# Optimization experiments

Hardware: AMD Instinct MI355X
Metric: run time of the kernel (lower is better)

Reference implementation:

```python
import jax, jax.numpy as jnp
import numpy as np

N = 50000      # total nodes
E = 800000     # total edges (before self-loops)
B = 512        # graphs in batch
H = 4          # attention heads
D = 64         # per-head dim (hidden 256 = H*D)
F_IN = 203     # node feature dim
HID = H * D
NEG_SLOPE = 0.2  # PyG GATConv LeakyReLU default
LN_EPS = 1e-5


def setup_inputs() -> dict:
    key = jax.random.key(0)
    ks = jax.random.split(key, 24)
    g = lambda k, shape, fan: (jax.random.normal(k, shape, jnp.float32) / np.sqrt(fan))
    inp = {
        "x": jax.random.normal(ks[0], (N, F_IN), jnp.float32),
        "edge_index": jax.random.randint(ks[1], (2, E), 0, N, jnp.int64),
        "edge_weight": jax.random.uniform(ks[2], (E,), jnp.float32),
        "batch": jnp.sort(jax.random.randint(ks[3], (N,), 0, B, jnp.int64)),
        # GAT layer 1 params
        "W1": g(ks[4], (HID, F_IN), F_IN),
        "a_s1": g(ks[5], (H, D), D),
        "a_d1": g(ks[6], (H, D), D),
        "a_e1": g(ks[7], (H, D), D),
        "We1": g(ks[8], (HID, 1), 1),
        "b1": jnp.zeros((HID,), jnp.float32),
        # GAT layer 2 params
        "W2": g(ks[9], (HID, HID), HID),
        "a_s2": g(ks[10], (H, D), D),
        "a_d2": g(ks[11], (H, D), D),
        "a_e2": g(ks[12], (H, D), D),
        "We2": g(ks[13], (HID, 1), 1),
        "b2": jnp.zeros((HID,), jnp.float32),
        # LayerNorms
        "ln1_g": jnp.ones((HID,), jnp.float32),
        "ln1_b": jnp.zeros((HID,), jnp.float32),
        "ln2_g": jnp.ones((HID,), jnp.float32),
        "ln2_b": jnp.zeros((HID,), jnp.float32),
    }
    return inp


def _gat(x, src, dst, e_attr, W, a_s, a_d, a_e, We, bias, n_nodes):
    # projected node features: [N, H, D]
    xp = (x @ W.T).reshape(n_nodes, H, D)
    alpha_src = jnp.einsum('nhd,hd->nh', xp, a_s)   # [N, H]
    alpha_dst = jnp.einsum('nhd,hd->nh', xp, a_d)   # [N, H]
    ep = (e_attr @ We.T).reshape(-1, H, D)          # [E', H, D]
    alpha_edge = jnp.einsum('ehd,hd->eh', ep, a_e)  # [E', H]
    logits = jax.nn.leaky_relu(alpha_src[src] + alpha_dst[dst] + alpha_edge, NEG_SLOPE)
    # segment softmax over incoming edges per destination node
    m = jax.ops.segment_max(logits, dst, num_segments=n_nodes)
    ex = jnp.exp(logits - m[dst])
    denom = jax.ops.segment_sum(ex, dst, num_segments=n_nodes)
    alpha = ex / denom[dst]                          # [E', H]
    msg = alpha[:, :, None] * xp[src]                # [E', H, D]
    out = jax.ops.segment_sum(msg, dst, num_segments=n_nodes)
    return out.reshape(n_nodes, HID) + bias


def _ln(x, g, b):
    mu = x.mean(-1, keepdims=True)
    var = ((x - mu) ** 2).mean(-1, keepdims=True)
    return (x - mu) * jax.lax.rsqrt(var + LN_EPS) * g + b


def reference(x, edge_index, edge_weight, batch,
              W1, a_s1, a_d1, a_e1, We1, b1,
              W2, a_s2, a_d2, a_e2, We2, b2,
              ln1_g, ln1_b, ln2_g, ln2_b):
    n = x.shape[0]
    # PyG GATConv add_self_loops=True, edge_attr fill_value='mean'
    loop = jnp.arange(n)
    src = jnp.concatenate([edge_index[0], loop])
    dst = jnp.concatenate([edge_index[1], loop])
    ew = jnp.concatenate([edge_weight, jnp.full((n,), edge_weight.mean(), edge_weight.dtype)])
    e_attr = ew[:, None]  # edge_dim = 1

    h = _gat(x, src, dst, e_attr, W1, a_s1, a_d1, a_e1, We1, b1, n)
    h = jax.nn.elu(_ln(h, ln1_g, ln1_b))  # dropout omitted (eval mode)
    h = _gat(h, src, dst, e_attr, W2, a_s2, a_d2, a_e2, We2, b2, n)
    h = jax.nn.elu(_ln(h, ln2_g, ln2_b))

    # global_mean_pool
    s = jax.ops.segment_sum(h, batch, num_segments=B)
    cnt = jax.ops.segment_sum(jnp.ones((n,), h.dtype), batch, num_segments=B)
    return s / jnp.maximum(cnt, 1.0)[:, None]
```

## Files before the change

kernel.cpp:

```cpp
#include <hip/hip_runtime.h>
#include <math.h>

#define HID 256
#define NEG_SLOPE 0.2f
#define LN_EPS 1e-5f
#define BINCAP 127

typedef __attribute__((ext_vector_type(4))) float f32x4;
typedef __attribute__((ext_vector_type(8))) short bf16x8;
typedef __attribute__((address_space(3))) unsigned char lds_b;
typedef const __attribute__((address_space(1))) unsigned char glob_b;

__device__ __forceinline__ float bf2f_lo(unsigned int u) {
    union { unsigned int i; float f; } c; c.i = u << 16; return c.f;
}
__device__ __forceinline__ float bf2f_hi(unsigned int u) {
    union { unsigned int i; float f; } c; c.i = u & 0xffff0000u; return c.f;
}
__device__ __forceinline__ float bf2f_u(unsigned short u) {
    union { unsigned int i; float f; } c; c.i = ((unsigned int)u) << 16; return c.f;
}
__device__ __forceinline__ unsigned short f2bf(float f) {
    union { float f; unsigned int i; } c; c.f = f;
    unsigned int i = c.i;
    return (unsigned short)((i + 0x7fffu + ((i >> 16) & 1u)) >> 16);
}

__global__ __launch_bounds__(256) void k_pre(const float* __restrict__ ew, int E,
                                             const int* __restrict__ ei, int N, int EN, int NH,
                                             float* __restrict__ partials,
                                             int* __restrict__ bins, int* __restrict__ spill, int* __restrict__ spill_cnt,
                                             const float* __restrict__ W1, const float* __restrict__ W2,
                                             unsigned short* __restrict__ o1, unsigned short* __restrict__ o2, int K1,
                                             const float* __restrict__ x, unsigned short* __restrict__ x16, int FIN) {
    int t = threadIdx.x;
    int b = blockIdx.x;
    if (b < NH) {
        int i = b * 1024 + t;
#pragma unroll
        for (int c = 0; c < 4; c++) {
            int e = i + c * 256;
            if (e < EN) {
                int d = (e < E) ? ei[E + e] : (e - E);
                int* row = bins + (size_t)d * 128;
                int pos = atomicAdd(row, 1);
                if (pos < BINCAP) row[1 + pos] = e;
                else { int q = atomicAdd(spill_cnt, 1); spill[2 * q] = d; spill[2 * q + 1] = e; }
            }
        }
    } else if (b < NH + 256) {
        __shared__ float sdata[4];
        int sb = b - NH;
        float v = 0.f;
        for (int i = sb * 256 + t; i < E; i += 65536) v += ew[i];
        for (int o = 32; o; o >>= 1) v += __shfl_xor(v, o);
        if ((t & 63) == 0) sdata[t >> 6] = v;
        __syncthreads();
        if (t == 0) partials[sb] = sdata[0] + sdata[1] + sdata[2] + sdata[3];
    } else if (b < NH + 256 + 512) {
        int wb = b - NH - 256;
        const float* in = (wb < 256) ? W1 : W2;
        unsigned short* out = (wb < 256) ? o1 : o2;
        int K = (wb < 256) ? K1 : 256;
        int col = wb & 255;
        float v = (t < K) ? in[(size_t)col * K + t] : 0.f;
        int ks = t >> 5, j = (t >> 3) & 3, e = t & 7;
        out[ks * 8192 + j * 2048 + ((((col << 4) ^ (j << 4))) >> 1) + e] = f2bf(v);
    } else {
        int r = b - NH - 256 - 512;
        x16[(size_t)r * 256 + t] = (t < FIN) ? f2bf(x[(size_t)r * FIN + t]) : (unsigned short)0;
    }
}

__global__ __launch_bounds__(256) void k_scanred_coeff(const int* __restrict__ bins, int N, int NB,
                                                       int* __restrict__ deg_dense, int* __restrict__ bsum,
                                                       const float* __restrict__ partials, float* __restrict__ sumw,
                                                       const float* __restrict__ We1, const float* __restrict__ ae1,
                                                       const float* __restrict__ We2, const float* __restrict__ ae2,
                                                       float* __restrict__ c1, float* __restrict__ c2) {
    int t = threadIdx.x;
    int b = blockIdx.x;
    if (b < NB) {
        __shared__ int sdata[4];
        int i = b * 256 + t;
        int v = (i < N) ? bins[(size_t)i * 128] : 0;
        if (i < N) deg_dense[i] = v;
        for (int o = 32; o; o >>= 1) v += __shfl_xor(v, o);
        if ((t & 63) == 0) sdata[t >> 6] = v;
        __syncthreads();
        if (t == 0) bsum[b] = sdata[0] + sdata[1] + sdata[2] + sdata[3];
    } else if (b == NB) {
        __shared__ float sdata[4];
        float v = partials[t];
        for (int o = 32; o; o >>= 1) v += __shfl_xor(v, o);
        if ((t & 63) == 0) sdata[t >> 6] = v;
        __syncthreads();
        if (t == 0) *sumw = sdata[0] + sdata[1] + sdata[2] + sdata[3];
    } else {
        float v1 = We1[t] * ae1[t];
        float v2 = We2[t] * ae2[t];
        for (int o = 1; o < 64; o <<= 1) { v1 += __shfl_xor(v1, o); v2 += __shfl_xor(v2, o); }
        if ((t & 63) == 0) { c1[t >> 6] = v1; c2[t >> 6] = v2; }
    }
}

__global__ __launch_bounds__(256) void k_scan_apply(const int* __restrict__ deg, int N, int NB,
                                                    const int* __restrict__ bsum, int* __restrict__ offs) {
    __shared__ int sm[256];
    __shared__ int sb[256];
    int t = threadIdx.x;
    int i = blockIdx.x * 256 + t;
    int v = (i < N) ? deg[i] : 0;
    int vb = (t < NB) ? bsum[t] : 0;
    sm[t] = v;
    sb[t] = vb;
    __syncthreads();
    for (int o = 1; o < 256; o <<= 1) {
        int tv = (t >= o) ? sm[t - o] : 0;
        int tb = (t >= o) ? sb[t - o] : 0;
        __syncthreads();
        sm[t] += tv;
        sb[t] += tb;
        __syncthreads();
    }
    int myb = bsum[blockIdx.x];
    int boff = sb[blockIdx.x] - myb;
    if (i < N) {
        offs[i] = boff + sm[t] - v;
        if (i == N - 1) offs[N] = boff + sm[t];
    }
}

__device__ __forceinline__ void gemm_dev(int bid,
    const unsigned short* __restrict__ A16, const unsigned short* __restrict__ Bt16, int M,
    const float* __restrict__ asf, const float* __restrict__ adf,
    unsigned short* __restrict__ C16, float* __restrict__ as_out, float* __restrict__ ad_out)
{
    __shared__ __align__(16) unsigned short Bsl[4 * 256 * 8];
    int t = threadIdx.x;
    int lane = t & 63, w = t >> 6;
    int row0 = bid << 5;
    int kg = lane >> 4, fr = lane & 15;

    int ar0 = row0 + fr;      if (ar0 >= M) ar0 = 0;
    int ar1 = row0 + 16 + fr; if (ar1 >= M) ar1 = 0;
    const unsigned short* ap0 = A16 + (size_t)ar0 * 256 + (kg << 3);
    const unsigned short* ap1 = A16 + (size_t)ar1 * 256 + (kg << 3);

    f32x4 acc[2][4];
#pragma unroll
    for (int i = 0; i < 2; i++)
#pragma unroll
        for (int j = 0; j < 4; j++) acc[i][j] = (f32x4){0.f, 0.f, 0.f, 0.f};

    for (int ks = 0; ks < 8; ks++) {
#pragma unroll
        for (int j = 0; j < 4; j++) {
            __builtin_amdgcn_global_load_lds(
                (glob_b*)(Bt16 + (size_t)ks * 8192 + j * 2048 + t * 8),
                (lds_b*)((char*)Bsl + j * 4096 + t * 16),
                16, 0, 0);
        }
        bf16x8 a0 = *(const bf16x8*)(ap0 + (ks << 5));
        bf16x8 a1 = *(const bf16x8*)(ap1 + (ks << 5));
        __syncthreads();
#pragma unroll
        for (int nf = 0; nf < 4; nf++) {
            int col = (w << 6) + (nf << 4) + fr;
            bf16x8 bv = *(const bf16x8*)((const char*)Bsl + (kg << 12) + (((col << 4)) ^ (kg << 4)));
            acc[0][nf] = __builtin_amdgcn_mfma_f32_16x16x32_bf16(a0, bv, acc[0][nf], 0, 0, 0);
            acc[1][nf] = __builtin_amdgcn_mfma_f32_16x16x32_bf16(a1, bv, acc[1][nf], 0, 0, 0);
        }
        __syncthreads();
    }

#pragma unroll
    for (int mf = 0; mf < 2; mf++)
#pragma unroll
        for (int j = 0; j < 4; j++) {
            int gr = row0 + mf * 16 + kg * 4 + j;
            if (gr < M) {
#pragma unroll
                for (int nf = 0; nf < 4; nf++)
                    C16[(size_t)gr * 256 + (w << 6) + (nf << 4) + fr] = f2bf(acc[mf][nf][j]);
            }
        }
    float asv[4], adv[4];
#pragma unroll
    for (int nf = 0; nf < 4; nf++) {
        int col = (w << 6) + (nf << 4) + fr;
        asv[nf] = asf[col]; adv[nf] = adf[col];
    }
#pragma unroll
    for (int mf = 0; mf < 2; mf++)
#pragma unroll
        for (int j = 0; j < 4; j++) {
            float ps = acc[mf][0][j] * asv[0] + acc[mf][1][j] * asv[1] + acc[mf][2][j] * asv[2] + acc[mf][3][j] * asv[3];
            float pd = acc[mf][0][j] * adv[0] + acc[mf][1][j] * adv[1] + acc[mf][2][j] * adv[2] + acc[mf][3][j] * adv[3];
#pragma unroll
            for (int o = 1; o < 16; o <<= 1) { ps += __shfl_xor(ps, o); pd += __shfl_xor(pd, o); }
            if (fr == 0) {
                int gr = row0 + mf * 16 + kg * 4 + j;
                if (gr < M) {
                    as_out[gr * 4 + w] = ps;
                    ad_out[gr * 4 + w] = pd;
                }
            }
        }
}

__device__ __forceinline__ void compact_dev(int bid, const int* __restrict__ offs,
                                            const int* __restrict__ bins,
                                            const int* __restrict__ spill, const int* __restrict__ spill_cnt,
                                            const int* __restrict__ ei, const float* __restrict__ ew,
                                            const float* __restrict__ sumw, int E, int N,
                                            int* __restrict__ csr_src, float* __restrict__ csr_w) {
    int lane = threadIdx.x & 63;
    int n = (bid << 2) + (threadIdx.x >> 6);
    if (n >= N) return;
    int s0 = offs[n];
    int d = offs[n + 1] - s0;
    if (d <= 0) return;
    if (d <= 64) {
        int key = (lane < d) ? bins[(size_t)n * 128 + 1 + lane] : 0x7fffffff;
        int rank = 0;
        for (int j = 0; j < d; j++) {
            int kj = __shfl(key, j);
            rank += (kj < key) ? 1 : 0;
        }
        if (lane < d) {
            int s; float wv;
            if (key < E) { s = ei[key]; wv = ew[key]; }
            else         { s = key - E; wv = *sumw / (float)E; }
            csr_src[s0 + rank] = s;
            csr_w[s0 + rank] = wv;
        }
    } else {
        if (lane == 0) {
            int m = (d < BINCAP) ? d : BINCAP;
            for (int i = 0; i < m; i++) csr_src[s0 + i] = bins[(size_t)n * 128 + 1 + i];
            int cnt = m;
            int st = *spill_cnt;
            for (int k = 0; k < st; k++)
                if (spill[2 * k] == n) csr_src[s0 + cnt++] = spill[2 * k + 1];
            for (int i = s0 + 1; i < s0 + d; i++) {
                int ke = csr_src[i];
                int j = i - 1;
                while (j >= s0 && csr_src[j] > ke) { csr_src[j + 1] = csr_src[j]; j--; }
                csr_src[j + 1] = ke;
            }
        }
        __threadfence();
        __builtin_amdgcn_wave_barrier();
        for (int i = lane; i < d; i += 64) {
            int e = csr_src[s0 + i];
            int s; float wv;
            if (e < E) { s = ei[e]; wv = ew[e]; }
            else       { s = e - E; wv = *sumw / (float)E; }
            csr_src[s0 + i] = s;
            csr_w[s0 + i] = wv;
        }
    }
}

__global__ __launch_bounds__(256) void k_gemm_sort(int MB,
    const unsigned short* __restrict__ A16, const unsigned short* __restrict__ Bt16, int M,
    const float* __restrict__ asf, const float* __restrict__ adf,
    unsigned short* __restrict__ C16, float* __restrict__ as_out, float* __restrict__ ad_out,
    const int* __restrict__ offs, const int* __restrict__ bins,
    const int* __restrict__ spill, const int* __restrict__ spill_cnt,
    const int* __restrict__ ei, const float* __restrict__ ew,
    const float* __restrict__ sumw, int E,
    int* __restrict__ csr_src, float* __restrict__ csr_w) {
    if ((int)blockIdx.x < MB)
        gemm_dev(blockIdx.x, A16, Bt16, M, asf, adf, C16, as_out, ad_out);
    else
        compact_dev(blockIdx.x - MB, offs, bins, spill, spill_cnt, ei, ew, sumw, E, M, csr_src, csr_w);
}

__global__ __launch_bounds__(256) void gemm_mfma(
    const unsigned short* __restrict__ A16, const unsigned short* __restrict__ Bt16, int M,
    const float* __restrict__ asf, const float* __restrict__ adf,
    unsigned short* __restrict__ C16, float* __restrict__ as_out, float* __restrict__ ad_out) {
    gemm_dev(blockIdx.x, A16, Bt16, M, asf, adf, C16, as_out, ad_out);
}

#define ACC8V(u, q) do { \
    f32x4 va = { bf2f_lo((u).x), bf2f_hi((u).x), bf2f_lo((u).y), bf2f_hi((u).y) }; \
    f32x4 vb = { bf2f_lo((u).z), bf2f_hi((u).z), bf2f_lo((u).w), bf2f_hi((u).w) }; \
    accA += va * (q); accB += vb * (q); } while (0)

__global__ __launch_bounds__(256) void gat_kernel(
    const unsigned short* __restrict__ xp16, const int* __restrict__ offs,
    const int* __restrict__ csr_src, const float* __restrict__ csr_w,
    const float* __restrict__ as_, const float* __restrict__ ad_,
    const float* __restrict__ cvec, const float* __restrict__ bias,
    const float* __restrict__ ln_g, const float* __restrict__ ln_b,
    int N, unsigned short* __restrict__ out16) {
    __shared__ float p_lds[4][256];
    __shared__ int   s_lds[4][64];
    int lane = threadIdx.x & 63;
    int wid = threadIdx.x >> 6;
    int n = (blockIdx.x << 2) + wid;
    if (n >= N) return;
    int start = offs[n], end = offs[n + 1];
    int e0 = lane >> 5;
    int colb = lane & 31;
    int hq2 = colb >> 3;
    const unsigned short* xbase = xp16 + (size_t)colb * 8;
    float4 adv = *(const float4*)(ad_ + (size_t)n * 4);
    float c0 = cvec[0], c1 = cvec[1], c2 = cvec[2], c3 = cvec[3];
    float dn = 0.f;
    f32x4 accA = (f32x4){0.f, 0.f, 0.f, 0.f};
    f32x4 accB = (f32x4){0.f, 0.f, 0.f, 0.f};

    for (int base = start; base < end; base += 64) {
        int idx = base + lane;
        bool act = idx < end;
        int s = act ? csr_src[idx] : 0;
        float w = act ? csr_w[idx] : 0.f;
        float4 av = *(const float4*)(as_ + (size_t)s * 4);
        float l0 = av.x + adv.x + w * c0; l0 = l0 >= 0.f ? l0 : NEG_SLOPE * l0;
        float l1 = av.y + adv.y + w * c1; l1 = l1 >= 0.f ? l1 : NEG_SLOPE * l1;
        float l2 = av.z + adv.z + w * c2; l2 = l2 >= 0.f ? l2 : NEG_SLOPE * l2;
        float l3 = av.w + adv.w + w * c3; l3 = l3 >= 0.f ? l3 : NEG_SLOPE * l3;
        float p0 = act ? __expf(fminf(l0, 80.f)) : 0.f;
        float p1 = act ? __expf(fminf(l1, 80.f)) : 0.f;
        float p2 = act ? __expf(fminf(l2, 80.f)) : 0.f;
        float p3 = act ? __expf(fminf(l3, 80.f)) : 0.f;
        float4 pv = { p0, p1, p2, p3 };
        *(float4*)&p_lds[wid][lane << 2] = pv;
        s_lds[wid][lane] = s;
        int cnt = end - base; if (cnt > 64) cnt = 64;
        int k = 0;
        for (; k + 8 <= cnt; k += 8) {
            int i0 = k + e0, i1 = k + 2 + e0, i2 = k + 4 + e0, i3 = k + 6 + e0;
            int s0 = s_lds[wid][i0], s1 = s_lds[wid][i1], s2 = s_lds[wid][i2], s3 = s_lds[wid][i3];
            uint4 u0 = *(const uint4*)(xbase + (size_t)s0 * 256);
            uint4 u1 = *(const uint4*)(xbase + (size_t)s1 * 256);
            uint4 u2 = *(const uint4*)(xbase + (size_t)s2 * 256);
            uint4 u3 = *(const uint4*)(xbase + (size_t)s3 * 256);
            float q0 = p_lds[wid][(i0 << 2) + hq2];
            float q1 = p_lds[wid][(i1 << 2) + hq2];
            float q2 = p_lds[wid][(i2 << 2) + hq2];
            float q3 = p_lds[wid][(i3 << 2) + hq2];
            dn += q0 + q1 + q2 + q3;
            ACC8V(u0, q0); ACC8V(u1, q1); ACC8V(u2, q2); ACC8V(u3, q3);
        }
        for (; k < cnt; k += 2) {
            int i = k + e0;
            bool v = i < cnt;
            int si = s_lds[wid][v ? i : 0];
            float qi = v ? p_lds[wid][(i << 2) + hq2] : 0.f;
            uint4 u = *(const uint4*)(xbase + (size_t)si * 256);
            dn += qi;
            ACC8V(u, qi);
        }
    }
#pragma unroll
    for (int o = 32; o == 32; o = 0) {
        accA[0] += __shfl_xor(accA[0], 32); accA[1] += __shfl_xor(accA[1], 32);
        accA[2] += __shfl_xor(accA[2], 32); accA[3] += __shfl_xor(accA[3], 32);
        accB[0] += __shfl_xor(accB[0], 32); accB[1] += __shfl_xor(accB[1], 32);
        accB[2] += __shfl_xor(accB[2], 32); accB[3] += __shfl_xor(accB[3], 32);
        dn += __shfl_xor(dn, 32);
    }
    float inv = 1.f / dn;
    int cb8 = colb << 3;
    float4 bA = *(const float4*)(bias + cb8);
    float4 bB = *(const float4*)(bias + cb8 + 4);
    float o0 = accA[0] * inv + bA.x, o1 = accA[1] * inv + bA.y, o2 = accA[2] * inv + bA.z, o3 = accA[3] * inv + bA.w;
    float o4 = accB[0] * inv + bB.x, o5 = accB[1] * inv + bB.y, o6 = accB[2] * inv + bB.z, o7 = accB[3] * inv + bB.w;
    float part = ((o0 + o1) + (o2 + o3)) + ((o4 + o5) + (o6 + o7));
    for (int o = 16; o; o >>= 1) part += __shfl_xor(part, o);
    float mu = part * (1.f / 256.f);
    float d0 = o0 - mu, d1 = o1 - mu, d2 = o2 - mu, d3 = o3 - mu;
    float d4 = o4 - mu, d5 = o5 - mu, d6 = o6 - mu, d7 = o7 - mu;
    float vpart = ((d0 * d0 + d1 * d1) + (d2 * d2 + d3 * d3)) + ((d4 * d4 + d5 * d5) + (d6 * d6 + d7 * d7));
    for (int o = 16; o; o >>= 1) vpart += __shfl_xor(vpart, o);
    float rstd = rsqrtf(vpart * (1.f / 256.f) + LN_EPS);
    float4 gA = *(const float4*)(ln_g + cb8), gB = *(const float4*)(ln_g + cb8 + 4);
    float4 eA = *(const float4*)(ln_b + cb8), eB = *(const float4*)(ln_b + cb8 + 4);
    float y0 = d0 * rstd * gA.x + eA.x; y0 = y0 > 0.f ? y0 : __expf(y0) - 1.f;
    float y1 = d1 * rstd * gA.y + eA.y; y1 = y1 > 0.f ? y1 : __expf(y1) - 1.f;
    float y2 = d2 * rstd * gA.z + eA.z; y2 = y2 > 0.f ? y2 : __expf(y2) - 1.f;
    float y3 = d3 * rstd * gA.w + eA.w; y3 = y3 > 0.f ? y3 : __expf(y3) - 1.f;
    float y4 = d4 * rstd * gB.x + eB.x; y4 = y4 > 0.f ? y4 : __expf(y4) - 1.f;
    float y5 = d5 * rstd * gB.y + eB.y; y5 = y5 > 0.f ? y5 : __expf(y5) - 1.f;
    float y6 = d6 * rstd * gB.z + eB.z; y6 = y6 > 0.f ? y6 : __expf(y6) - 1.f;
    float y7 = d7 * rstd * gB.w + eB.w; y7 = y7 > 0.f ? y7 : __expf(y7) - 1.f;
    if (lane < 32) {
        uint4 ov;
        ov.x = ((unsigned int)f2bf(y1) << 16) | f2bf(y0);
        ov.y = ((unsigned int)f2bf(y3) << 16) | f2bf(y2);
        ov.z = ((unsigned int)f2bf(y5) << 16) | f2bf(y4);
        ov.w = ((unsigned int)f2bf(y7) << 16) | f2bf(y6);
        *(uint4*)(out16 + (size_t)n * HID + cb8) = ov;
    }
}

__device__ __forceinline__ int lower_bound_i(const int* a, int n, int key) {
    int lo = 0, hi = n;
    while (lo < hi) { int mid = (lo + hi) >> 1; if (a[mid] < key) lo = mid + 1; else hi = mid; }
    return lo;
}

__global__ __launch_bounds__(256) void pool_kernel(const unsigned short* __restrict__ h, const int* __restrict__ batch,
                                                   int N, float* __restrict__ out) {
    int b = blockIdx.x;
    int lo = lower_bound_i(batch, N, b);
    int hi = lower_bound_i(batch, N, b + 1);
    float a0 = 0.f, a1 = 0.f, a2 = 0.f, a3 = 0.f;
    int n = lo;
    for (; n + 4 <= hi; n += 4) {
        a0 += bf2f_u(h[(size_t)(n + 0) * HID + threadIdx.x]);
        a1 += bf2f_u(h[(size_t)(n + 1) * HID + threadIdx.x]);
        a2 += bf2f_u(h[(size_t)(n + 2) * HID + threadIdx.x]);
        a3 += bf2f_u(h[(size_t)(n + 3) * HID + threadIdx.x]);
    }
    for (; n < hi; n++) a0 += bf2f_u(h[(size_t)n * HID + threadIdx.x]);
    float acc = (a0 + a1) + (a2 + a3);
    out[(size_t)b * HID + threadIdx.x] = acc / fmaxf((float)(hi - lo), 1.f);
}

extern "C" void kernel_launch(void* const* d_in, const int* in_sizes, int n_in,
                              void* d_out, int out_size, void* d_ws, size_t ws_size,
                              hipStream_t stream) {
    const float* x    = (const float*)d_in[0];
    const int*   ei   = (const int*)d_in[1];
    const float* ew   = (const float*)d_in[2];
    const int*   batch= (const int*)d_in[3];
    const float* W1   = (const float*)d_in[4];
    const float* as1  = (const float*)d_in[5];
    const float* ad1  = (const float*)d_in[6];
    const float* ae1  = (const float*)d_in[7];
    const float* We1  = (const float*)d_in[8];
    const float* b1   = (const float*)d_in[9];
    const float* W2   = (const float*)d_in[10];
    const float* as2  = (const float*)d_in[11];
    const float* ad2  = (const float*)d_in[12];
    const float* ae2  = (const float*)d_in[13];
    const float* We2  = (const float*)d_in[14];
    const float* b2   = (const float*)d_in[15];
    const float* ln1g = (const float*)d_in[16];
    const float* ln1b = (const float*)d_in[17];
    const float* ln2g = (const float*)d_in[18];
    const float* ln2b = (const float*)d_in[19];

    int N = in_sizes[3];
    int E = in_sizes[2];
    int FIN = in_sizes[0] / N;
    int EN = E + N;
    int B = out_size / HID;
    float* outp = (float*)d_out;
    int NB = (N + 255) / 256;
    int NH = (EN + 1023) / 1024;

    char* ws = (char*)d_ws;
    size_t off = 0;
    auto alloc = [&](size_t bytes) { void* p = ws + off; off = (off + bytes + 255) & ~(size_t)255; return p; };
    float* sumw      = (float*)alloc(4);
    int*   spill_cnt = (int*)  alloc(4);
    int*   bins      = (int*)  alloc((size_t)N * 128 * 4);
    size_t zero_bytes = 512 + (size_t)N * 128 * 4;
    float* partials= (float*)alloc(256 * 4);
    int*   bsum    = (int*)  alloc(256 * 4);
    int*   deg     = (int*)  alloc((size_t)N * 4);
    int*   offs    = (int*)  alloc((size_t)(N + 1) * 4);
    int*   spill   = (int*)  alloc((size_t)EN * 2 * 4);
    int*   csr_src = (int*)  alloc((size_t)EN * 4);
    float* csr_w   = (float*)alloc((size_t)EN * 4);
    float* asb     = (float*)alloc((size_t)N * 4 * 4);
    float* adb     = (float*)alloc((size_t)N * 4 * 4);
    float* cc      = (float*)alloc(64);
    unsigned short* w1_16 = (unsigned short*)alloc((size_t)HID * HID * 2);
    unsigned short* w2_16 = (unsigned short*)alloc((size_t)HID * HID * 2);
    unsigned short* x16   = (unsigned short*)alloc((size_t)N * HID * 2);
    unsigned short* xp16  = (unsigned short*)alloc((size_t)N * HID * 2);
    (void)ws_size; (void)n_in;

    int MB = (N + 31) / 32;
    int NC = (N + 3) / 4;

    (void)hipMemsetAsync(d_ws, 0, zero_bytes, stream);
    k_pre<<<NH + 256 + 512 + N, 256, 0, stream>>>(ew, E, ei, N, EN, NH, partials,
                                                  bins, spill, spill_cnt,
                                                  W1, W2, w1_16, w2_16, FIN, x, x16, FIN);
    k_scanred_coeff<<<NB + 2, 256, 0, stream>>>(bins, N, NB, deg, bsum, partials, sumw, We1, ae1, We2, ae2, cc, cc + 4);
    k_scan_apply<<<NB, 256, 0, stream>>>(deg, N, NB, bsum, offs);
    k_gemm_sort<<<MB + NC, 256, 0, stream>>>(MB, x16, w1_16, N, as1, ad1, xp16, asb, adb,
                                             offs, bins, spill, spill_cnt, ei, ew, sumw, E, csr_src, csr_w);
    gat_kernel<<<NC, 256, 0, stream>>>(xp16, offs, csr_src, csr_w, asb, adb, cc, b1, ln1g, ln1b, N, x16);
    gemm_mfma<<<MB, 256, 0, stream>>>(x16, w2_16, N, as2, ad2, xp16, asb, adb);
    gat_kernel<<<NC, 256, 0, stream>>>(xp16, offs, csr_src, csr_w, asb, adb, cc + 4, b2, ln2g, ln2b, N, x16);
    pool_kernel<<<B, 256, 0, stream>>>(x16, batch, N, outp);
}
```

Measured before the change: 303.9 us.

## Move layer-1 GEMM into preprocessing kernel alongside edge binning

Converting x and W1 to bf16 now happens in two separate small kernels launched first. The layer-1 GEMM then runs inside k_pre next to the edge binning, edge-weight reduction and W2 conversion, instead of sharing a kernel with CSR compaction. Compaction becomes its own kernel. The aim is to overlap the GEMM with the atomic-heavy binning work. The cost is two extra launches and some serialization, since compaction no longer overlaps anything. The W1/W2 conversion branch in k_pre now writes W2 twice, which is redundant work.

```diff
diff --git a/kernel.cpp b/kernel.cpp
--- a/kernel.cpp
+++ b/kernel.cpp
@@ -26,13 +26,100 @@
     return (unsigned short)((i + 0x7fffu + ((i >> 16) & 1u)) >> 16);
 }
 
-__global__ __launch_bounds__(256) void k_pre(const float* __restrict__ ew, int E,
-                                             const int* __restrict__ ei, int N, int EN, int NH,
+__global__ __launch_bounds__(256) void k_cvt(const float* __restrict__ in, unsigned short* __restrict__ out, int K) {
+    int r = blockIdx.x, t = threadIdx.x;
+    out[(size_t)r * 256 + t] = (t < K) ? f2bf(in[(size_t)r * K + t]) : (unsigned short)0;
+}
+
+__device__ __forceinline__ void gemm_dev(int bid,
+    const unsigned short* __restrict__ A16, const unsigned short* __restrict__ Bt16, int M,
+    const float* __restrict__ asf, const float* __restrict__ adf,
+    unsigned short* __restrict__ C16, float* __restrict__ as_out, float* __restrict__ ad_out)
+{
+    __shared__ __align__(16) unsigned short Bsl[4 * 256 * 8];
+    int t = threadIdx.x;
+    int lane = t & 63, w = t >> 6;
+    int row0 = bid << 5;
+    int kg = lane >> 4, fr = lane & 15;
+
+    int ar0 = row0 + fr;      if (ar0 >= M) ar0 = 0;
+    int ar1 = row0 + 16 + fr; if (ar1 >= M) ar1 = 0;
+    const unsigned short* ap0 = A16 + (size_t)ar0 * 256 + (kg << 3);
+    const unsigned short* ap1 = A16 + (size_t)ar1 * 256 + (kg << 3);
+
+    f32x4 acc[2][4];
+#pragma unroll
+    for (int i = 0; i < 2; i++)
+#pragma unroll
+        for (int j = 0; j < 4; j++) acc[i][j] = (f32x4){0.f, 0.f, 0.f, 0.f};
+
+    for (int ks = 0; ks < 8; ks++) {
+#pragma unroll
+        for (int j = 0; j < 4; j++) {
+            __builtin_amdgcn_global_load_lds(
+                (glob_b*)(Bt16 + (size_t)ks * 8192 + j * 2048 + t * 8),
+                (lds_b*)((char*)Bsl + j * 4096 + t * 16),
+                16, 0, 0);
+        }
+        bf16x8 a0 = *(const bf16x8*)(ap0 + (ks << 5));
+        bf16x8 a1 = *(const bf16x8*)(ap1 + (ks << 5));
+        __syncthreads();
+#pragma unroll
+        for (int nf = 0; nf < 4; nf++) {
+            int col = (w << 6) + (nf << 4) + fr;
+            bf16x8 bv = *(const bf16x8*)((const char*)Bsl + (kg << 12) + (((col << 4)) ^ (kg << 4)));
+            acc[0][nf] = __builtin_amdgcn_mfma_f32_16x16x32_bf16(a0, bv, acc[0][nf], 0, 0, 0);
+            acc[1][nf] = __builtin_amdgcn_mfma_f32_16x16x32_bf16(a1, bv, acc[1][nf], 0, 0, 0);
+        }
+        __syncthreads();
+    }
+
+#pragma unroll
+    for (int mf = 0; mf < 2; mf++)
+#pragma unroll
+        for (int j = 0; j < 4; j++) {
+            int gr = row0 + mf * 16 + kg * 4 + j;
+            if (gr < M) {
+#pragma unroll
+                for (int nf = 0; nf < 4; nf++)
+                    C16[(size_t)gr * 256 + (w << 6) + (nf << 4) + fr] = f2bf(acc[mf][nf][j]);
+            }
+        }
+    float asv[4], adv[4];
+#pragma unroll
+    for (int nf = 0; nf < 4; nf++) {
+        int col = (w << 6) + (nf << 4) + fr;
+        asv[nf] = asf[col]; adv[nf] = adf[col];
+    }
+#pragma unroll
+    for (int mf = 0; mf < 2; mf++)
+#pragma unroll
+        for (int j = 0; j < 4; j++) {
+            float ps = acc[mf][0][j] * asv[0] + acc[mf][1][j] * asv[1] + acc[mf][2][j] * asv[2] + acc[mf][3][j] * asv[3];
+            float pd = acc[mf][0][j] * adv[0] + acc[mf][1][j] * adv[1] + acc[mf][2][j] * adv[2] + acc[mf][3][j] * adv[3];
+#pragma unroll
+            for (int o = 1; o < 16; o <<= 1) { ps += __shfl_xor(ps, o); pd += __shfl_xor(pd, o); }
+            if (fr == 0) {
+                int gr = row0 + mf * 16 + kg * 4 + j;
+                if (gr < M) {
+                    as_out[gr * 4 + w] = ps;
+                    ad_out[gr * 4 + w] = pd;
+                }
+            }
+        }
+}
+
+__global__ __launch_bounds__(256) void k_pre(int NH, int MB,
+                                             const float* __restrict__ ew, int E,
+                                             const int* __restrict__ ei, int N, int EN,
                                              float* __restrict__ partials,
                                              int* __restrict__ bins, int* __restrict__ spill, int* __restrict__ spill_cnt,
                                              const float* __restrict__ W1, const float* __restrict__ W2,
                                              unsigned short* __restrict__ o1, unsigned short* __restrict__ o2, int K1,
-                                             const float* __restrict__ x, unsigned short* __restrict__ x16, int FIN) {
+                                             const unsigned short* __restrict__ x16,
+                                             const float* __restrict__ asf, const float* __restrict__ adf,
+                                             unsigned short* __restrict__ xp16,
+                                             float* __restrict__ asb, float* __restrict__ adb) {
     int t = threadIdx.x;
     int b = blockIdx.x;
     if (b < NH) {
@@ -48,28 +135,37 @@
                 else { int q = atomicAdd(spill_cnt, 1); spill[2 * q] = d; spill[2 * q + 1] = e; }
             }
         }
-    } else if (b < NH + 256) {
+    } else if (b < NH + MB) {
+        gemm_dev(b - NH, x16, o1, N, asf, adf, xp16, asb, adb);
+    } else if (b < NH + MB + 256) {
         __shared__ float sdata[4];
-        int sb = b - NH;
+        int sb = b - NH - MB;
         float v = 0.f;
         for (int i = sb * 256 + t; i < E; i += 65536) v += ew[i];
         for (int o = 32; o; o >>= 1) v += __shfl_xor(v, o);
         if ((t & 63) == 0) sdata[t >> 6] = v;
         __syncthreads();
         if (t == 0) partials[sb] = sdata[0] + sdata[1] + sdata[2] + sdata[3];
-    } else if (b < NH + 256 + 512) {
-        int wb = b - NH - 256;
+    } else {
+        int wb = b - NH - MB - 256;
         const float* in = (wb < 256) ? W1 : W2;
         unsigned short* out = (wb < 256) ? o1 : o2;
-        int K = (wb < 256) ? K1 : 256;
+        int K = 256;
         int col = wb & 255;
+        if (wb < 256) { in = W2; out = o2; }
+        else          { in = W2; out = o2; }
+        (void)K1;
         float v = (t < K) ? in[(size_t)col * K + t] : 0.f;
         int ks = t >> 5, j = (t >> 3) & 3, e = t & 7;
         out[ks * 8192 + j * 2048 + ((((col << 4) ^ (j << 4))) >> 1) + e] = f2bf(v);
-    } else {
-        int r = b - NH - 256 - 512;
-        x16[(size_t)r * 256 + t] = (t < FIN) ? f2bf(x[(size_t)r * FIN + t]) : (unsigned short)0;
-    }
+    }
+}
+
+__global__ __launch_bounds__(256) void k_cvt_w1(const float* __restrict__ W1, unsigned short* __restrict__ o1, int K1) {
+    int col = blockIdx.x, k = threadIdx.x;
+    float v = (k < K1) ? W1[(size_t)col * K1 + k] : 0.f;
+    int ks = k >> 5, j = (k >> 3) & 3, e = k & 7;
+    o1[ks * 8192 + j * 2048 + ((((col << 4) ^ (j << 4))) >> 1) + e] = f2bf(v);
 }
 
 __global__ __launch_bounds__(256) void k_scanred_coeff(const int* __restrict__ bins, int N, int NB,
@@ -131,92 +227,14 @@
     }
 }
 
-__device__ __forceinline__ void gemm_dev(int bid,
-    const unsigned short* __restrict__ A16, const unsigned short* __restrict__ Bt16, int M,
-    const float* __restrict__ asf, const float* __restrict__ adf,
-    unsigned short* __restrict__ C16, float* __restrict__ as_out, float* __restrict__ ad_out)
-{
-    __shared__ __align__(16) unsigned short Bsl[4 * 256 * 8];
-    int t = threadIdx.x;
-    int lane = t & 63, w = t >> 6;
-    int row0 = bid << 5;
-    int kg = lane >> 4, fr = lane & 15;
-
-    int ar0 = row0 + fr;      if (ar0 >= M) ar0 = 0;
-    int ar1 = row0 + 16 + fr; if (ar1 >= M) ar1 = 0;
-    const unsigned short* ap0 = A16 + (size_t)ar0 * 256 + (kg << 3);
-    const unsigned short* ap1 = A16 + (size_t)ar1 * 256 + (kg << 3);
-
-    f32x4 acc[2][4];
-#pragma unroll
-    for (int i = 0; i < 2; i++)
-#pragma unroll
-        for (int j = 0; j < 4; j++) acc[i][j] = (f32x4){0.f, 0.f, 0.f, 0.f};
-
-    for (int ks = 0; ks < 8; ks++) {
-#pragma unroll
-        for (int j = 0; j < 4; j++) {
-            __builtin_amdgcn_global_load_lds(
-                (glob_b*)(Bt16 + (size_t)ks * 8192 + j * 2048 + t * 8),
-                (lds_b*)((char*)Bsl + j * 4096 + t * 16),
-                16, 0, 0);
-        }
-        bf16x8 a0 = *(const bf16x8*)(ap0 + (ks << 5));
-        bf16x8 a1 = *(const bf16x8*)(ap1 + (ks << 5));
-        __syncthreads();
-#pragma unroll
-        for (int nf = 0; nf < 4; nf++) {
-            int col = (w << 6) + (nf << 4) + fr;
-            bf16x8 bv = *(const bf16x8*)((const char*)Bsl + (kg << 12) + (((col << 4)) ^ (kg << 4)));
-            acc[0][nf] = __builtin_amdgcn_mfma_f32_16x16x32_bf16(a0, bv, acc[0][nf], 0, 0, 0);
-            acc[1][nf] = __builtin_amdgcn_mfma_f32_16x16x32_bf16(a1, bv, acc[1][nf], 0, 0, 0);
-        }
-        __syncthreads();
-    }
-
-#pragma unroll
-    for (int mf = 0; mf < 2; mf++)
-#pragma unroll
-        for (int j = 0; j < 4; j++) {
-            int gr = row0 + mf * 16 + kg * 4 + j;
-            if (gr < M) {
-#pragma unroll
-                for (int nf = 0; nf < 4; nf++)
-                    C16[(size_t)gr * 256 + (w << 6) + (nf << 4) + fr] = f2bf(acc[mf][nf][j]);
-            }
-        }
-    float asv[4], adv[4];
-#pragma unroll
-    for (int nf = 0; nf < 4; nf++) {
-        int col = (w << 6) + (nf << 4) + fr;
-        asv[nf] = asf[col]; adv[nf] = adf[col];
-    }
-#pragma unroll
-    for (int mf = 0; mf < 2; mf++)
-#pragma unroll
-        for (int j = 0; j < 4; j++) {
-            float ps = acc[mf][0][j] * asv[0] + acc[mf][1][j] * asv[1] + acc[mf][2][j] * asv[2] + acc[mf][3][j] * asv[3];
-            float pd = acc[mf][0][j] * adv[0] + acc[mf][1][j] * adv[1] + acc[mf][2][j] * adv[2] + acc[mf][3][j] * adv[3];
-#pragma unroll
-            for (int o = 1; o < 16; o <<= 1) { ps += __shfl_xor(ps, o); pd += __shfl_xor(pd, o); }
-            if (fr == 0) {
-                int gr = row0 + mf * 16 + kg * 4 + j;
-                if (gr < M) {
-                    as_out[gr * 4 + w] = ps;
-                    ad_out[gr * 4 + w] = pd;
-                }
-            }
-        }
-}
-
-__device__ __forceinline__ void compact_dev(int bid, const int* __restrict__ offs,
-                                            const int* __restrict__ bins,
-                                            const int* __restrict__ spill, const int* __restrict__ spill_cnt,
-                                            const int* __restrict__ ei, const float* __restrict__ ew,
-                                            const float* __restrict__ sumw, int E, int N,
-                                            int* __restrict__ csr_src, float* __restrict__ csr_w) {
+__global__ __launch_bounds__(256) void k_compact(const int* __restrict__ offs,
+                                                 const int* __restrict__ bins,
+                                                 const int* __restrict__ spill, const int* __restrict__ spill_cnt,
+                                                 const int* __restrict__ ei, const float* __restrict__ ew,
+                                                 const float* __restrict__ sumw, int E, int N,
+                                                 int* __restrict__ csr_src, float* __restrict__ csr_w) {
     int lane = threadIdx.x & 63;
-    int n = (bid << 2) + (threadIdx.x >> 6);
+    int n = ((int)blockIdx.x << 2) + (threadIdx.x >> 6);
     if (n >= N) return;
     int s0 = offs[n];
     int d = offs[n + 1] - s0;
@@ -261,21 +279,6 @@
             csr_w[s0 + i] = wv;
         }
     }
-}
-
-__global__ __launch_bounds__(256) void k_gemm_sort(int MB,
-    const unsigned short* __restrict__ A16, const unsigned short* __restrict__ Bt16, int M,
-    const float* __restrict__ asf, const float* __restrict__ adf,
-    unsigned short* __restrict__ C16, float* __restrict__ as_out, float* __restrict__ ad_out,
-    const int* __restrict__ offs, const int* __restrict__ bins,
-    const int* __restrict__ spill, const int* __restrict__ spill_cnt,
-    const int* __restrict__ ei, const float* __restrict__ ew,
-    const float* __restrict__ sumw, int E,
-    int* __restrict__ csr_src, float* __restrict__ csr_w) {
-    if ((int)blockIdx.x < MB)
-        gemm_dev(blockIdx.x, A16, Bt16, M, asf, adf, C16, as_out, ad_out);
-    else
-        compact_dev(blockIdx.x - MB, offs, bins, spill, spill_cnt, ei, ew, sumw, E, M, csr_src, csr_w);
 }
 
 __global__ __launch_bounds__(256) void gemm_mfma(
@@ -357,14 +360,11 @@
             ACC8V(u, qi);
         }
     }
-#pragma unroll
-    for (int o = 32; o == 32; o = 0) {
-        accA[0] += __shfl_xor(accA[0], 32); accA[1] += __shfl_xor(accA[1], 32);
-        accA[2] += __shfl_xor(accA[2], 32); accA[3] += __shfl_xor(accA[3], 32);
-        accB[0] += __shfl_xor(accB[0], 32); accB[1] += __shfl_xor(accB[1], 32);
-        accB[2] += __shfl_xor(accB[2], 32); accB[3] += __shfl_xor(accB[3], 32);
-        dn += __shfl_xor(dn, 32);
-    }
+    accA[0] += __shfl_xor(accA[0], 32); accA[1] += __shfl_xor(accA[1], 32);
+    accA[2] += __shfl_xor(accA[2], 32); accA[3] += __shfl_xor(accA[3], 32);
+    accB[0] += __shfl_xor(accB[0], 32); accB[1] += __shfl_xor(accB[1], 32);
+    accB[2] += __shfl_xor(accB[2], 32); accB[3] += __shfl_xor(accB[3], 32);
+    dn += __shfl_xor(dn, 32);
     float inv = 1.f / dn;
     int cb8 = colb << 3;
     float4 bA = *(const float4*)(bias + cb8);
@@ -483,13 +483,15 @@
     int NC = (N + 3) / 4;
 
     (void)hipMemsetAsync(d_ws, 0, zero_bytes, stream);
-    k_pre<<<NH + 256 + 512 + N, 256, 0, stream>>>(ew, E, ei, N, EN, NH, partials,
-                                                  bins, spill, spill_cnt,
-                                                  W1, W2, w1_16, w2_16, FIN, x, x16, FIN);
+    k_cvt<<<N, 256, 0, stream>>>(x, x16, FIN);
+    k_cvt_w1<<<HID, 256, 0, stream>>>(W1, w1_16, FIN);
+    k_pre<<<NH + MB + 256 + 512, 256, 0, stream>>>(NH, MB, ew, E, ei, N, EN, partials,
+                                                   bins, spill, spill_cnt,
+                                                   W1, W2, w1_16, w2_16, FIN,
+                                                   x16, as1, ad1, xp16, asb, adb);
     k_scanred_coeff<<<NB + 2, 256, 0, stream>>>(bins, N, NB, deg, bsum, partials, sumw, We1, ae1, We2, ae2, cc, cc + 4);
     k_scan_apply<<<NB, 256, 0, stream>>>(deg, N, NB, bsum, offs);
-    k_gemm_sort<<<MB + NC, 256, 0, stream>>>(MB, x16, w1_16, N, as1, ad1, xp16, asb, adb,
-                                             offs, bins, spill, spill_cnt, ei, ew, sumw, E, csr_src, csr_w);
+    k_compact<<<NC, 256, 0, stream>>>(offs, bins, spill, spill_cnt, ei, ew, sumw, E, N, csr_src, csr_w);
     gat_kernel<<<NC, 256, 0, stream>>>(xp16, offs, csr_src, csr_w, asb, adb, cc, b1, ln1g, ln1b, N, x16);
     gemm_mfma<<<MB, 256, 0, stream>>>(x16, w2_16, N, as2, ad2, xp16, asb, adb);
     gat_kernel<<<NC, 256, 0, stream>>>(xp16, offs, csr_src, csr_w, asb, adb, cc + 4, b2, ln2g, ln2b, N, x16);
```

New measurement: 307.8 us. Within noise of the previous version (+1.3%).
